# Kernel tuning notes

Measured on AMD Instinct MI355X. Metric: run time of the kernel, lower is better.

Reference implementation:

```python
import jax, jax.numpy as jnp
import numpy as np

# Model dims (match init_kwargs)
HID = 1024   # hidden_size
H   = 16     # num_heads
DK  = 64     # head_dim (key)
DV  = 128    # head value dim = int(head_dim * expand_v)
VAL = H * DV # value_dim = 2048
CONV = 4     # short conv kernel size
EPS = 1e-6
NORM_EPS = 1e-5


def _causal_conv_silu(x, w):
    # x: [B,T,C], w: [C,K] depthwise causal conv, no bias, silu activation
    T = x.shape[1]
    K = w.shape[1]
    xp = jnp.pad(x, ((0, 0), (K - 1, 0), (0, 0)))
    y = sum(xp[:, i:i + T, :] * w[:, i] for i in range(K))
    return jax.nn.silu(y)


def setup_inputs() -> dict:
    key = jax.random.key(0)
    ks = jax.random.split(key, 16)
    s = 0.02
    rn = lambda k, sh: jax.random.normal(k, sh, jnp.float32)
    return {
        'hidden_states': rn(ks[0], (1, 2048, HID)),
        'norm_w': jnp.ones((HID,), jnp.float32),
        'q_w': rn(ks[1], (H * DK, HID)) * s,
        'k_w': rn(ks[2], (H * DK, HID)) * s,
        'v_w': rn(ks[3], (VAL, HID)) * s,
        'a_w': rn(ks[4], (H, HID)) * s,
        'b_w': rn(ks[5], (H, HID)) * s,
        'g_w': rn(ks[6], (VAL, HID)) * s,
        'dt_bias': jax.random.uniform(ks[7], (H,), jnp.float32, -2.0, 0.0),
        'A_log': jnp.log(jax.random.uniform(ks[8], (H,), jnp.float32, 1.0, 8.0)),
        'conv_q_w': rn(ks[9], (H * DK, CONV)) * 0.2,
        'conv_k_w': rn(ks[10], (H * DK, CONV)) * 0.2,
        'conv_v_w': rn(ks[11], (VAL, CONV)) * 0.2,
        'o_norm_w': jnp.ones((DV,), jnp.float32),
        'o_proj_w': rn(ks[12], (HID, VAL)) * s,
        'out_proj_w': rn(ks[13], (HID, HID)) * s,
    }


def reference(hidden_states, norm_w, q_w, k_w, v_w, a_w, b_w, g_w, dt_bias,
              A_log, conv_q_w, conv_k_w, conv_v_w, o_norm_w, o_proj_w, out_proj_w):
    B, T, D = hidden_states.shape
    # RMSNorm
    x = hidden_states * jax.lax.rsqrt(
        jnp.mean(hidden_states * hidden_states, -1, keepdims=True) + EPS) * norm_w

    # projections + causal depthwise short conv + silu
    q = _causal_conv_silu(x @ q_w.T, conv_q_w).reshape(B, T, H, DK)
    k = _causal_conv_silu(x @ k_w.T, conv_k_w).reshape(B, T, H, DK)
    v = _causal_conv_silu(x @ v_w.T, conv_v_w).reshape(B, T, H, DV)

    beta = jax.nn.sigmoid(x @ b_w.T)                       # [B,T,H]
    g = -jnp.exp(A_log) * jax.nn.softplus(x @ a_w.T + dt_bias)  # [B,T,H] log-decay

    # rank-1 DC removal on keys: (I - 1 1^T / DK) k, i.e. subtract per-head mean
    k = k - jnp.mean(k, -1, keepdims=True)

    # L2 normalize q, k along head dim; scale q
    q = q * jax.lax.rsqrt(jnp.sum(q * q, -1, keepdims=True) + EPS)
    k = k * jax.lax.rsqrt(jnp.sum(k * k, -1, keepdims=True) + EPS)
    q = q * (DK ** -0.5)

    # gated delta-rule recurrence over time (time-major scan)
    qT = q.transpose(1, 0, 2, 3)
    kT = k.transpose(1, 0, 2, 3)
    vT = v.transpose(1, 0, 2, 3)
    bT = beta.transpose(1, 0, 2)
    gT = g.transpose(1, 0, 2)

    def step(S, inp):
        qt, kt, vt, bt, gt = inp              # S: [B,H,DK,DV]
        S = S * jnp.exp(gt)[..., None, None]
        v_new = (vt - jnp.einsum('bhk,bhkv->bhv', kt, S)) * bt[..., None]
        S = S + jnp.einsum('bhk,bhv->bhkv', kt, v_new)
        o = jnp.einsum('bhk,bhkv->bhv', qt, S)
        return S, o

    S0 = jnp.zeros((B, H, DK, DV), x.dtype)
    _, oT = jax.lax.scan(step, S0, (qT, kT, vT, bT, gT))
    o = oT.transpose(1, 0, 2, 3)                           # [B,T,H,DV]

    # gated RMSNorm on output heads
    gate = (x @ g_w.T).reshape(B, T, H, DV)
    o = o * jax.lax.rsqrt(jnp.mean(o * o, -1, keepdims=True) + NORM_EPS) * o_norm_w
    o = o * jax.nn.silu(gate)

    o = o.reshape(B, T, VAL) @ o_proj_w.T                  # [B,T,HID]
    return o @ out_proj_w.T
```

## Files before the change

kernel.cpp:

```cpp
#include <hip/hip_runtime.h>
#include <math.h>

#define S72 72

typedef __bf16 bf16;
typedef __bf16 bf16x8 __attribute__((ext_vector_type(8)));
typedef __bf16 bf16x4v __attribute__((ext_vector_type(4)));
typedef __bf16 bf16x2v __attribute__((ext_vector_type(2)));
typedef float f32x4 __attribute__((ext_vector_type(4)));

__device__ __forceinline__ float wredsum(float v) {
#pragma unroll
  for (int off = 32; off > 0; off >>= 1) v += __shfl_xor(v, off, 64);
  return v;
}
__device__ __forceinline__ float sigmoidf_(float x) { return 1.f / (1.f + __expf(-x)); }

__device__ __forceinline__ int sxy(int row, int col) {
  return (row << 6) + ((((col >> 3) ^ (row & 7)) << 3) | (col & 7));
}
__device__ __forceinline__ int sx8(int row, int chunk) {
  return (row << 6) + ((chunk ^ (row & 7)) << 3);
}

__global__ __launch_bounds__(256) void k_pre(const float* __restrict__ h,
    const float* __restrict__ nw, const float* __restrict__ aw,
    const float* __restrict__ bw, const float* __restrict__ dtb,
    const float* __restrict__ alog, bf16* __restrict__ xb,
    float* __restrict__ graw, float* __restrict__ btb,
    const float* __restrict__ qw, const float* __restrict__ kw,
    const float* __restrict__ vw, const float* __restrict__ gw,
    const float* __restrict__ opw, const float* __restrict__ ow,
    bf16* qwb, bf16* kwb, bf16* vwb, bf16* gwb, bf16* opwb, bf16* owb) {
  __shared__ float red[4];
  __shared__ __align__(16) float xs[1024];
  int tid = threadIdx.x;
  if (blockIdx.x >= 2048) {
    long cb = blockIdx.x - 2048;
    for (long u = cb*256 + tid; u < 2359296; u += 4608l*256) {
      const float* src; bf16* dst; long l;
      if      (u <  262144) { src=qw;  dst=qwb;  l=u; }
      else if (u <  524288) { src=kw;  dst=kwb;  l=u-262144; }
      else if (u < 1048576) { src=vw;  dst=vwb;  l=u-524288; }
      else if (u < 1572864) { src=gw;  dst=gwb;  l=u-1048576; }
      else if (u < 2097152) { src=opw; dst=opwb; l=u-1572864; }
      else                  { src=ow;  dst=owb;  l=u-2097152; }
      float4 s = *(const float4*)(src + l*4);
      bf16x4v b; b[0]=(bf16)s.x; b[1]=(bf16)s.y; b[2]=(bf16)s.z; b[3]=(bf16)s.w;
      *(bf16x4v*)(dst + l*4) = b;
    }
    return;
  }
  int t = blockIdx.x;
  float4 hv = *(const float4*)(h + (size_t)t*1024 + tid*4);
  float ss = hv.x*hv.x + hv.y*hv.y + hv.z*hv.z + hv.w*hv.w;
  float wsum = wredsum(ss);
  if ((tid & 63) == 0) red[tid >> 6] = wsum;
  __syncthreads();
  float tot = red[0] + red[1] + red[2] + red[3];
  float rs = rsqrtf(tot * (1.f/1024.f) + 1e-6f);
  float4 w4 = *(const float4*)(nw + tid*4);
  float4 y;
  y.x = hv.x*rs*w4.x; y.y = hv.y*rs*w4.y; y.z = hv.z*rs*w4.z; y.w = hv.w*rs*w4.w;
  *(float4*)(xs + tid*4) = y;
  bf16x4v b; b[0]=(bf16)y.x; b[1]=(bf16)y.y; b[2]=(bf16)y.z; b[3]=(bf16)y.w;
  *(bf16x4v*)(xb + (size_t)t*1024 + tid*4) = b;
  __syncthreads();
  int wave = tid >> 6, lane = tid & 63;
  const float4* x4 = (const float4*)xs;
#pragma unroll
  for (int hi = 0; hi < 4; ++hi) {
    int hh = wave*4 + hi;
    float sa = 0.f, sb = 0.f;
#pragma unroll
    for (int i = 0; i < 4; ++i) {
      float4 xv = x4[i*64 + lane];
      float4 av = *(const float4*)(aw + hh*1024 + i*256 + lane*4);
      float4 bv = *(const float4*)(bw + hh*1024 + i*256 + lane*4);
      sa += xv.x*av.x + xv.y*av.y + xv.z*av.z + xv.w*av.w;
      sb += xv.x*bv.x + xv.y*bv.y + xv.z*bv.z + xv.w*bv.w;
    }
    sa = wredsum(sa); sb = wredsum(sb);
    if (lane == 0) {
      float ap = sa + dtb[hh];
      float sp = (ap > 20.f) ? ap : log1pf(expf(ap));
      graw[t*16 + hh] = -expf(alog[hh]) * sp;
      btb[t*16 + hh] = 1.f / (1.f + expf(-sb));
    }
  }
}

template <typename OutT>
__device__ __forceinline__ void gemm_body(const bf16* __restrict__ A,
    const bf16* __restrict__ B, OutT* __restrict__ C, int N, int K, int m0, int n0) {
  __shared__ bf16 As[2][128*32];
  __shared__ bf16 Bs[2][128*32];
  const int tid = threadIdx.x, lane = tid & 63, wave = tid >> 6;
  const int wm = (wave >> 1) * 64, wn = (wave & 1) * 64;
  const int srow = wave*16 + (lane >> 2);
  const int swl = (((lane & 3) ^ ((lane >> 3) & 3))) * 8;
  const int sdst = (lane & 3) * 8;
  const int quad = lane >> 4, l16 = lane & 15;
  const int sw = (l16 >> 1) & 3;
  f32x4 acc[4][4] = {};
  const int nk = K >> 5;
#pragma unroll
  for (int i = 0; i < 2; ++i) {
    int r = i*64 + srow;
    __builtin_amdgcn_global_load_lds(
      (__attribute__((address_space(1))) void*)(A + (size_t)(m0 + r)*K + swl),
      (__attribute__((address_space(3))) void*)(&As[0][r*32 + sdst]), 16, 0, 0);
    __builtin_amdgcn_global_load_lds(
      (__attribute__((address_space(1))) void*)(B + (size_t)(n0 + r)*K + swl),
      (__attribute__((address_space(3))) void*)(&Bs[0][r*32 + sdst]), 16, 0, 0);
  }
  for (int kt = 0; kt < nk; ++kt) {
    const int cur = kt & 1;
    __syncthreads();
    bf16x8 af[4], bfr[4];
#pragma unroll
    for (int mt = 0; mt < 4; ++mt)
      af[mt] = *(const bf16x8*)(&As[cur][(wm + mt*16 + l16)*32 + (quad ^ sw)*8]);
#pragma unroll
    for (int nt = 0; nt < 4; ++nt)
      bfr[nt] = *(const bf16x8*)(&Bs[cur][(wn + nt*16 + l16)*32 + (quad ^ sw)*8]);
    if (kt + 1 < nk) {
      int k0 = (kt + 1) << 5;
#pragma unroll
      for (int i = 0; i < 2; ++i) {
        int r = i*64 + srow;
        __builtin_amdgcn_global_load_lds(
          (__attribute__((address_space(1))) void*)(A + (size_t)(m0 + r)*K + k0 + swl),
          (__attribute__((address_space(3))) void*)(&As[cur^1][r*32 + sdst]), 16, 0, 0);
        __builtin_amdgcn_global_load_lds(
          (__attribute__((address_space(1))) void*)(B + (size_t)(n0 + r)*K + k0 + swl),
          (__attribute__((address_space(3))) void*)(&Bs[cur^1][r*32 + sdst]), 16, 0, 0);
      }
    }
#pragma unroll
    for (int mt = 0; mt < 4; ++mt)
#pragma unroll
      for (int nt = 0; nt < 4; ++nt)
        acc[mt][nt] = __builtin_amdgcn_mfma_f32_16x16x32_bf16(af[mt], bfr[nt], acc[mt][nt], 0, 0, 0);
  }
#pragma unroll
  for (int mt = 0; mt < 4; ++mt)
#pragma unroll
    for (int nt = 0; nt < 4; ++nt)
#pragma unroll
      for (int r = 0; r < 4; ++r) {
        int row = m0 + wm + mt*16 + quad*4 + r;
        int col = n0 + wn + nt*16 + l16;
        C[(size_t)row*N + col] = (OutT)acc[mt][nt][r];
      }
}

__global__ __launch_bounds__(256) void k_gemm_proj(const bf16* __restrict__ A,
    const bf16* __restrict__ qwb, const bf16* __restrict__ kwb,
    const bf16* __restrict__ vwb, const bf16* __restrict__ gwb,
    bf16* __restrict__ qpre, bf16* __restrict__ kpre,
    bf16* __restrict__ vpre, bf16* __restrict__ gpre) {
  int bx = blockIdx.x;
  const bf16* B; bf16* C; int N, xt;
  if      (bx <  8) { B = qwb; C = qpre; N = 1024; xt = bx; }
  else if (bx < 16) { B = kwb; C = kpre; N = 1024; xt = bx - 8; }
  else if (bx < 32) { B = vwb; C = vpre; N = 2048; xt = bx - 16; }
  else              { B = gwb; C = gpre; N = 2048; xt = bx - 32; }
  gemm_body<bf16>(A, B, C, N, 1024, blockIdx.y*128, xt*128);
}

template <typename OutT>
__global__ __launch_bounds__(256) void k_gemm_bt64(const bf16* __restrict__ A,
    const bf16* __restrict__ B, OutT* __restrict__ C, int N, int K) {
  __shared__ bf16 As[2][128*32];
  __shared__ bf16 Bs[2][64*32];
  const int tid = threadIdx.x, lane = tid & 63, wave = tid >> 6;
  const int wm = wave * 32;
  const int srow = wave*16 + (lane >> 2);
  const int swl = (((lane & 3) ^ ((lane >> 3) & 3))) * 8;
  const int sdst = (lane & 3) * 8;
  const int quad = lane >> 4, l16 = lane & 15;
  const int sw = (l16 >> 1) & 3;
  const int m0 = blockIdx.y * 128, n0 = blockIdx.x * 64;
  f32x4 acc[2][4] = {};
  const int nk = K >> 5;
#pragma unroll
  for (int i = 0; i < 2; ++i) {
    int r = i*64 + srow;
    __builtin_amdgcn_global_load_lds(
      (__attribute__((address_space(1))) void*)(A + (size_t)(m0 + r)*K + swl),
      (__attribute__((address_space(3))) void*)(&As[0][r*32 + sdst]), 16, 0, 0);
  }
  __builtin_amdgcn_global_load_lds(
    (__attribute__((address_space(1))) void*)(B + (size_t)(n0 + srow)*K + swl),
    (__attribute__((address_space(3))) void*)(&Bs[0][srow*32 + sdst]), 16, 0, 0);
  for (int kt = 0; kt < nk; ++kt) {
    const int cur = kt & 1;
    __syncthreads();
    bf16x8 af[2], bfr[4];
#pragma unroll
    for (int mt = 0; mt < 2; ++mt)
      af[mt] = *(const bf16x8*)(&As[cur][(wm + mt*16 + l16)*32 + (quad ^ sw)*8]);
#pragma unroll
    for (int nt = 0; nt < 4; ++nt)
      bfr[nt] = *(const bf16x8*)(&Bs[cur][(nt*16 + l16)*32 + (quad ^ sw)*8]);
    if (kt + 1 < nk) {
      int k0 = (kt + 1) << 5;
#pragma unroll
      for (int i = 0; i < 2; ++i) {
        int r = i*64 + srow;
        __builtin_amdgcn_global_load_lds(
          (__attribute__((address_space(1))) void*)(A + (size_t)(m0 + r)*K + k0 + swl),
          (__attribute__((address_space(3))) void*)(&As[cur^1][r*32 + sdst]), 16, 0, 0);
      }
      __builtin_amdgcn_global_load_lds(
        (__attribute__((address_space(1))) void*)(B + (size_t)(n0 + srow)*K + k0 + swl),
        (__attribute__((address_space(3))) void*)(&Bs[cur^1][srow*32 + sdst]), 16, 0, 0);
    }
#pragma unroll
    for (int mt = 0; mt < 2; ++mt)
#pragma unroll
      for (int nt = 0; nt < 4; ++nt)
        acc[mt][nt] = __builtin_amdgcn_mfma_f32_16x16x32_bf16(af[mt], bfr[nt], acc[mt][nt], 0, 0, 0);
  }
#pragma unroll
  for (int mt = 0; mt < 2; ++mt)
#pragma unroll
    for (int nt = 0; nt < 4; ++nt)
#pragma unroll
      for (int r = 0; r < 4; ++r) {
        int row = m0 + wm + mt*16 + quad*4 + r;
        int col = n0 + nt*16 + l16;
        C[(size_t)row*N + col] = (OutT)acc[mt][nt][r];
      }
}

template<int NT>
__device__ __forceinline__ void mm_band(const bf16* A_lds, const bf16* B_lds,
    int w16, int cb, int l16, int quad, f32x4* acc) {
#pragma unroll
  for (int n = 0; n < NT; ++n) { acc[n][0]=0.f; acc[n][1]=0.f; acc[n][2]=0.f; acc[n][3]=0.f; }
#pragma unroll
  for (int kt = 0; kt < 2; ++kt) {
    bf16x8 af = *(const bf16x8*)(A_lds + sx8(w16 + l16, kt*4 + quad));
#pragma unroll
    for (int n = 0; n < NT; ++n) {
      bf16x8 bf = *(const bf16x8*)(B_lds + sx8(cb + n*16 + l16, kt*4 + quad));
      acc[n] = __builtin_amdgcn_mfma_f32_16x16x32_bf16(af, bf, acc[n], 0, 0, 0);
    }
  }
}

__global__ __launch_bounds__(512, 4) void k_prepass(
    const bf16* __restrict__ qpre, const bf16* __restrict__ kpre,
    const bf16* __restrict__ vpre, const float* __restrict__ cqw,
    const float* __restrict__ ckw, const float* __restrict__ cvw,
    const float* __restrict__ graw, const float* __restrict__ beta,
    bf16* __restrict__ EF, float* __restrict__ dSl, float* __restrict__ obuf) {
  const int bx = blockIdx.x, c = bx >> 4, h = bx & 15, tid = threadIdx.x;
  const int t0 = c * 64;
  const int wave = tid >> 6, lane = tid & 63, l16 = lane & 15, quad = lane >> 4;
  const int w16 = (wave >> 1) * 16;
  const int chh = wave & 1;
  const int r0 = wave * 8;

  __shared__ bf16 SM[36864];
  __shared__ float bs[64], bts_s[64], es[64], gms[64];
  bf16* Kr    = SM;
  bf16* powR0 = SM + 4096;
  bf16* prod0 = SM + 8192;
  bf16* T2T   = SM + 12288;
  bf16* powT0 = SM + 16384;
  bf16* powR1 = SM + 20480;
  bf16* powT1 = SM + 24576;
  bf16* prod1 = SM + 28672;
  bf16* qbf   = SM + 32768;
  bf16* VT   = SM;
  bf16* VlT  = SM + 8192;
  bf16* KT   = powT0;
  bf16* KbT  = powR1;
  bf16* Pm   = powT1;
  bf16* WR   = prod0;
  bf16* Mrow = prod1;

  float4 wq  = *(const float4*)(cqw + (h*64 + lane)*4);
  float4 wk  = *(const float4*)(ckw + (h*64 + lane)*4);
  float4 wv0 = *(const float4*)(cvw + (h*128 + lane)*4);
  float4 wv1 = *(const float4*)(cvw + (h*128 + 64 + lane)*4);
  float qtv[11], ktv[11], vtv0[11], vtv1[11];
#pragma unroll
  for (int j = 0; j < 11; ++j) {
    int tg = t0 + r0 + j - 3;
    bool ok = tg >= 0;
    qtv[j]  = ok ? (float)qpre[(size_t)tg*1024 + h*64 + lane] : 0.f;
    ktv[j]  = ok ? (float)kpre[(size_t)tg*1024 + h*64 + lane] : 0.f;
    vtv0[j] = ok ? (float)vpre[(size_t)tg*2048 + h*128 + lane] : 0.f;
    vtv1[j] = ok ? (float)vpre[(size_t)tg*2048 + h*128 + 64 + lane] : 0.f;
  }

  if (tid < 64) {
    float g = graw[(size_t)(t0 + tid)*16 + h];
    float b = g;
#pragma unroll
    for (int off = 1; off < 64; off <<= 1) {
      float p = __shfl_up(b, off, 64);
      if (tid >= off) b += p;
    }
    bs[tid] = b;
    bts_s[tid] = beta[(size_t)(t0 + tid)*16 + h];
    float b63 = __shfl(b, 63, 64);
    es[tid] = __expf(b63 - b);
    gms[tid] = __expf(b);
  }

  float kreg[8], vreg[16];
  {
#pragma unroll
    for (int rr = 0; rr < 8; ++rr) {
      float y = qtv[rr]*wq.x + qtv[rr+1]*wq.y + qtv[rr+2]*wq.z + qtv[rr+3]*wq.w;
      y = y * sigmoidf_(y);
      float ssq = wredsum(y*y);
      y *= rsqrtf(ssq + 1e-6f) * 0.125f;
      qbf[sxy(r0+rr, lane)] = (bf16)y;
    }
#pragma unroll
    for (int rr = 0; rr < 8; ++rr) {
      float y = ktv[rr]*wk.x + ktv[rr+1]*wk.y + ktv[rr+2]*wk.z + ktv[rr+3]*wk.w;
      y = y * sigmoidf_(y);
      float s1 = y, s2 = y*y;
#pragma unroll
      for (int off = 32; off > 0; off >>= 1) {
        s1 += __shfl_xor(s1, off, 64);
        s2 += __shfl_xor(s2, off, 64);
      }
      float m = s1 * (1.f/64.f);
      float ssq = s2 - s1*m;
      y -= m;
      y *= rsqrtf(ssq + 1e-6f);
      kreg[rr] = y;
      Kr[sxy(r0+rr, lane)] = (bf16)y;
    }
#pragma unroll
    for (int rr = 0; rr < 8; ++rr) {
      float y0 = vtv0[rr]*wv0.x + vtv0[rr+1]*wv0.y + vtv0[rr+2]*wv0.z + vtv0[rr+3]*wv0.w;
      float y1 = vtv1[rr]*wv1.x + vtv1[rr+1]*wv1.y + vtv1[rr+2]*wv1.z + vtv1[rr+3]*wv1.w;
      vreg[rr]   = y0 * sigmoidf_(y0);
      vreg[8+rr] = y1 * sigmoidf_(y1);
    }
  }
  __syncthreads();

  {
    f32x4 acc[2];
    mm_band<2>(Kr, Kr, w16, chh*32, l16, quad, acc);
#pragma unroll
    for (int n = 0; n < 2; ++n) {
      int col = chh*32 + n*16 + l16;
      bf16x4v tv;
#pragma unroll
      for (int r = 0; r < 4; ++r) {
        int row = w16 + quad*4 + r;
        float nv = 0.f;
        if (row > col) nv = -bts_s[row] * __expf(bs[row] - bs[col]) * acc[n][r];
        bf16 nb = (bf16)nv;
        powR0[sxy(row, col)] = nb;
        tv[r] = nb;
        prod0[sxy(row, col)] = (row == col) ? (bf16)1.f : nb;
      }
      *(bf16x4v*)(powT0 + sxy(col, w16 + quad*4)) = tv;
    }
  }
  __syncthreads();

  int pc = 0, rc = 0;
#pragma unroll 1
  for (int i = 1; i <= 5; ++i) {
    bf16* sqA = pc ? powR1 : powR0;
    bf16* sqB = pc ? powT1 : powT0;
    bf16* sqRo = pc ? powR0 : powR1;
    bf16* sqTo = pc ? powT0 : powT1;
    {
      f32x4 acc[2];
      mm_band<2>(sqA, sqB, w16, chh*32, l16, quad, acc);
#pragma unroll
      for (int n = 0; n < 2; ++n) {
        int col = chh*32 + n*16 + l16;
        bf16x4v tv;
#pragma unroll
        for (int r = 0; r < 4; ++r) {
          int row = w16 + quad*4 + r;
          bf16 vb = (bf16)acc[n][r];
          sqRo[sxy(row, col)] = vb;
          tv[r] = vb;
        }
        *(bf16x4v*)(sqTo + sxy(col, w16 + quad*4)) = tv;
      }
    }
    __syncthreads();
    bf16* prA = rc ? prod1 : prod0;
    bf16* prO = rc ? prod0 : prod1;
    {
      f32x4 acc[2];
      mm_band<2>(prA, sqTo, w16, chh*32, l16, quad, acc);
#pragma unroll
      for (int n = 0; n < 2; ++n) {
        int col = chh*32 + n*16 + l16;
        bf16x4v tv;
#pragma unroll
        for (int r = 0; r < 4; ++r) {
          int row = w16 + quad*4 + r;
          float val = acc[n][r] + (float)prA[sxy(row, col)];
          prO[sxy(row, col)] = (bf16)val;
          tv[r] = (bf16)(val * bts_s[col] * gms[col]);
        }
        if (i == 5) *(bf16x4v*)(T2T + sxy(col, w16 + quad*4)) = tv;
      }
    }
    __syncthreads();
    pc ^= 1; rc ^= 1;
  }

#pragma unroll
  for (int rr = 0; rr < 8; ++rr) {
    KT[sxy(lane, r0+rr)]  = (bf16)kreg[rr];
    KbT[sxy(lane, r0+rr)] = (bf16)(kreg[rr] * es[r0+rr]);
  }
  {
    f32x4 acc[2];
#pragma unroll
    for (int n = 0; n < 2; ++n) { acc[n][0]=0.f; acc[n][1]=0.f; acc[n][2]=0.f; acc[n][3]=0.f; }
#pragma unroll
    for (int kt = 0; kt < 2; ++kt) {
      bf16x8 af = *(const bf16x8*)(qbf + sx8(w16 + l16, kt*4 + quad));
#pragma unroll
      for (int n = 0; n < 2; ++n) {
        bf16x8 bf = *(const bf16x8*)(Kr + sx8(chh*32 + n*16 + l16, kt*4 + quad));
        acc[n] = __builtin_amdgcn_mfma_f32_16x16x32_bf16(af, bf, acc[n], 0, 0, 0);
      }
    }
#pragma unroll
    for (int n = 0; n < 2; ++n) {
      int col = chh*32 + n*16 + l16;
#pragma unroll
      for (int r = 0; r < 4; ++r) {
        int row = w16 + quad*4 + r;
        float pv = (row >= col) ? __expf(bs[row] - bs[col]) * acc[n][r] : 0.f;
        Pm[sxy(row, col)] = (bf16)pv;
      }
    }
  }
  __syncthreads();

  {
    f32x4 acc[2];
    mm_band<2>(KbT, T2T, w16, chh*32, l16, quad, acc);
#pragma unroll
    for (int n = 0; n < 2; ++n) {
      int col = chh*32 + n*16 + l16;
#pragma unroll
      for (int r = 0; r < 4; ++r)
        WR[sxy(w16 + quad*4 + r, col)] = (bf16)acc[n][r];
    }
  }
#pragma unroll
  for (int hf = 0; hf < 2; ++hf)
#pragma unroll
    for (int rr = 0; rr < 8; ++rr)
      VT[sxy(hf*64 + lane, r0+rr)] = (bf16)(bts_s[r0+rr] * vreg[hf*8+rr]);
  __syncthreads();
  {
    f32x4 acc[2];
    mm_band<2>(WR, KT, w16, chh*32, l16, quad, acc);
    float gC = gms[63];
    size_t eb = (size_t)bx * 13824;
#pragma unroll
    for (int n = 0; n < 2; ++n) {
      int col = chh*32 + n*16 + l16;
#pragma unroll
      for (int r = 0; r < 4; ++r) {
        int row = w16 + quad*4 + r;
        float ev = ((row == col) ? gC : 0.f) - acc[n][r];
        bf16 eh = (bf16)ev;
        EF[eb + row*S72 + col] = eh;
        EF[eb + 4608 + row*S72 + col] = (bf16)(ev - (float)eh);
      }
    }
  }
  __syncthreads();
  {
    f32x4 acc[2];
    mm_band<2>(Pm, T2T, w16, chh*32, l16, quad, acc);
#pragma unroll
    for (int n = 0; n < 2; ++n) {
      int col = chh*32 + n*16 + l16;
#pragma unroll
      for (int r = 0; r < 4; ++r)
        WR[sxy(w16 + quad*4 + r, col)] = (bf16)acc[n][r];
    }
  }
  __syncthreads();
  {
    f32x4 acc[2];
    mm_band<2>(WR, KT, w16, chh*32, l16, quad, acc);
    size_t eb = (size_t)bx * 13824;
#pragma unroll
    for (int n = 0; n < 2; ++n) {
      int col = chh*32 + n*16 + l16;
#pragma unroll
      for (int r = 0; r < 4; ++r) {
        int row = w16 + quad*4 + r;
        float qv = (float)qbf[sxy(row, col)];
        EF[eb + 9216 + row*S72 + col] = (bf16)(gms[row]*qv - acc[n][r]);
      }
    }
  }
  __syncthreads();
  {
    f32x4 acc[4];
    mm_band<4>(Mrow, VT, w16, chh*64, l16, quad, acc);
#pragma unroll
    for (int n = 0; n < 4; ++n) {
      int col = chh*64 + n*16 + l16;
      bf16x4v tv;
#pragma unroll
      for (int r = 0; r < 4; ++r) tv[r] = (bf16)acc[n][r];
      *(bf16x4v*)(VlT + sxy(col, w16 + quad*4)) = tv;
    }
  }
  __syncthreads();
  {
    f32x4 acc[4];
    mm_band<4>(KbT, VlT, w16, chh*64, l16, quad, acc);
#pragma unroll
    for (int n = 0; n < 4; ++n) {
      int col = chh*64 + n*16 + l16;
#pragma unroll
      for (int r = 0; r < 4; ++r)
        dSl[(size_t)bx*8192 + (size_t)(w16 + quad*4 + r)*128 + col] = acc[n][r];
    }
  }
  {
    f32x4 acc[4];
    mm_band<4>(Pm, VlT, w16, chh*64, l16, quad, acc);
#pragma unroll
    for (int n = 0; n < 4; ++n) {
      int col = chh*64 + n*16 + l16;
#pragma unroll
      for (int r = 0; r < 4; ++r)
        obuf[(size_t)(t0 + w16 + quad*4 + r)*2048 + h*128 + col] = acc[n][r];
    }
  }
}

#define SEQ_LOAD(Cn, EHx, ELx, FFx, DSx)                                        \
  {                                                                             \
    const bf16* base_ = EF + (size_t)((Cn)*16 + h)*13824 + arow;                \
    _Pragma("unroll")                                                           \
    for (int kt = 0; kt < 2; ++kt) {                                            \
      EHx[kt] = *(const bf16x8*)(base_ + kt*32);                                \
      ELx[kt] = *(const bf16x8*)(base_ + 4608 + kt*32);                         \
      FFx[kt] = *(const bf16x8*)(base_ + 9216 + kt*32);                         \
    }                                                                           \
    const float* db_ = dSl + (size_t)((Cn)*16 + h)*8192 + drow;                 \
    _Pragma("unroll")                                                           \
    for (int nt = 0; nt < 2; ++nt)                                              \
      _Pragma("unroll")                                                         \
      for (int r = 0; r < 4; ++r)                                               \
        DSx[nt*4+r] = db_[(size_t)r*128 + nt*16];                               \
  }

#define SEQ_STEP(Cc, EHc, ELc, FFc, DSc, EHn, ELn, FFn, DSn, SRC, DST)          \
  {                                                                             \
    bf16x8 bh[2][2], bl[2][2];                                                  \
    _Pragma("unroll")                                                           \
    for (int nt = 0; nt < 2; ++nt)                                              \
      _Pragma("unroll")                                                         \
      for (int kt = 0; kt < 2; ++kt) {                                          \
        bh[nt][kt] = *(const bf16x8*)(&Sthi[SRC][(nt*16 + l16)*S72 + kt*32 + quad*8]); \
        bl[nt][kt] = *(const bf16x8*)(&Stlo[SRC][(nt*16 + l16)*S72 + kt*32 + quad*8]); \
      }                                                                         \
    if ((Cc) + 1 < 32) SEQ_LOAD((Cc) + 1, EHn, ELn, FFn, DSn);                  \
    f32x4 a1[2], a2[2], a3[2], o1[2], o2[2];                                    \
    _Pragma("unroll")                                                           \
    for (int nt = 0; nt < 2; ++nt)                                              \
      _Pragma("unroll")                                                         \
      for (int r = 0; r < 4; ++r) {                                             \
        a1[nt][r] = DSc[nt*4+r];                                                \
        a2[nt][r] = 0.f; a3[nt][r] = 0.f; o1[nt][r] = 0.f; o2[nt][r] = 0.f;     \
      }                                                                         \
    _Pragma("unroll")                                                           \
    for (int kt = 0; kt < 2; ++kt)                                              \
      _Pragma("unroll")                                                         \
      for (int nt = 0; nt < 2; ++nt) {                                          \
        a1[nt] = __builtin_amdgcn_mfma_f32_16x16x32_bf16(EHc[kt], bh[nt][kt], a1[nt], 0, 0, 0); \
        a2[nt] = __builtin_amdgcn_mfma_f32_16x16x32_bf16(EHc[kt], bl[nt][kt], a2[nt], 0, 0, 0); \
        a3[nt] = __builtin_amdgcn_mfma_f32_16x16x32_bf16(ELc[kt], bh[nt][kt], a3[nt], 0, 0, 0); \
        o1[nt] = __builtin_amdgcn_mfma_f32_16x16x32_bf16(FFc[kt], bh[nt][kt], o1[nt], 0, 0, 0); \
        o2[nt] = __builtin_amdgcn_mfma_f32_16x16x32_bf16(FFc[kt], bl[nt][kt], o2[nt], 0, 0, 0); \
      }                                                                         \
    {                                                                           \
      int t0c = (Cc)*64;                                                        \
      _Pragma("unroll")                                                         \
      for (int nt = 0; nt < 2; ++nt)                                            \
        _Pragma("unroll")                                                       \
        for (int r = 0; r < 4; ++r)                                             \
          osb[(size_t)(t0c + mb + quad*4 + r)*2048 + h*128 + dq*32 + nt*16 + l16] \
            = o1[nt][r] + o2[nt][r];                                            \
    }                                                                           \
    _Pragma("unroll")                                                           \
    for (int nt = 0; nt < 2; ++nt) {                                            \
      bf16x4v hv, lv;                                                           \
      _Pragma("unroll")                                                         \
      for (int r = 0; r < 4; ++r) {                                             \
        float v = a1[nt][r] + a2[nt][r] + a3[nt][r];                            \
        bf16 hb = (bf16)v;                                                      \
        hv[r] = hb;                                                             \
        lv[r] = (bf16)(v - (float)hb);                                          \
      }                                                                         \
      *(bf16x4v*)(&Sthi[DST][(nt*16 + l16)*S72 + mb + quad*4]) = hv;            \
      *(bf16x4v*)(&Stlo[DST][(nt*16 + l16)*S72 + mb + quad*4]) = lv;            \
    }                                                                           \
    asm volatile("s_waitcnt lgkmcnt(0)" ::: "memory");                          \
    __builtin_amdgcn_s_barrier();                                               \
  }

__global__ __launch_bounds__(256) void k_seq(const bf16* __restrict__ EF,
    const float* __restrict__ dSl, float* __restrict__ osb) {
  const int bid = blockIdx.x;
  const int h = (bid & 7) + 8*((bid >> 3) & 1);
  const int dq = bid >> 4;
  const int tid = threadIdx.x, wave = tid >> 6, lane = tid & 63;
  const int l16 = lane & 15, quad = lane >> 4;
  const int mb = wave * 16;
  __shared__ bf16 Sthi[2][32*S72], Stlo[2][32*S72];
  for (int i = tid; i < 2304; i += 256) { Sthi[0][i] = (bf16)0.f; Stlo[0][i] = (bf16)0.f; }

  const size_t arow = (size_t)(mb + l16)*S72 + quad*8;
  const size_t drow = (size_t)dq*32 + (size_t)(mb + quad*4)*128 + l16;

  bf16x8 ehA[2], elA[2], ffA[2], ehB[2], elB[2], ffB[2];
  float dsA[8], dsB[8];

  SEQ_LOAD(0, ehA, elA, ffA, dsA);
  asm volatile("s_waitcnt lgkmcnt(0)" ::: "memory");
  __builtin_amdgcn_s_barrier();

#pragma unroll 1
  for (int c = 0; c < 32; c += 2) {
    SEQ_STEP(c,     ehA, elA, ffA, dsA, ehB, elB, ffB, dsB, 0, 1);
    SEQ_STEP(c + 1, ehB, elB, ffB, dsB, ehA, elA, ffA, dsA, 1, 0);
  }
}

__global__ __launch_bounds__(256) void k_gatenorm(const float* __restrict__ o,
    const float* __restrict__ os, const bf16* __restrict__ gpre,
    const float* __restrict__ onw, bf16* __restrict__ og) {
  int t = blockIdx.x, wave = threadIdx.x >> 6, lane = threadIdx.x & 63;
  float2 nw = *(const float2*)(onw + lane*2);
#pragma unroll
  for (int hi = 0; hi < 4; ++hi) {
    int hh = wave*4 + hi;
    size_t base = (size_t)t*2048 + hh*128 + lane*2;
    float2 o2 = *(const float2*)(o + base);
    float2 s2 = *(const float2*)(os + base);
    o2.x += s2.x; o2.y += s2.y;
    float ss = wredsum(o2.x*o2.x + o2.y*o2.y);
    float rs = rsqrtf(ss * (1.f/128.f) + 1e-5f);
    bf16x2v g2 = *(const bf16x2v*)(gpre + base);
    float g0 = (float)g2[0], g1 = (float)g2[1];
    float r0 = o2.x * rs * nw.x * (g0 * sigmoidf_(g0));
    float r1 = o2.y * rs * nw.y * (g1 * sigmoidf_(g1));
    bf16x2v b; b[0] = (bf16)r0; b[1] = (bf16)r1;
    *(bf16x2v*)(og + base) = b;
  }
}

extern "C" void kernel_launch(void* const* d_in, const int* in_sizes, int n_in,
                              void* d_out, int out_size, void* d_ws, size_t ws_size,
                              hipStream_t stream) {
  const float* hs   = (const float*)d_in[0];
  const float* nw   = (const float*)d_in[1];
  const float* qw   = (const float*)d_in[2];
  const float* kw   = (const float*)d_in[3];
  const float* vw   = (const float*)d_in[4];
  const float* aw   = (const float*)d_in[5];
  const float* bw   = (const float*)d_in[6];
  const float* gw   = (const float*)d_in[7];
  const float* dtb  = (const float*)d_in[8];
  const float* alog = (const float*)d_in[9];
  const float* cqw  = (const float*)d_in[10];
  const float* ckw  = (const float*)d_in[11];
  const float* cvw  = (const float*)d_in[12];
  const float* onw  = (const float*)d_in[13];
  const float* opw  = (const float*)d_in[14];
  const float* ow   = (const float*)d_in[15];
  float* out = (float*)d_out;

  char* p = (char*)d_ws;
  auto alloc = [&](size_t bytes) { char* r = p; p += (bytes + 255) & ~255ull; return r; };
  bf16*  xb    = (bf16*) alloc((size_t)2048*1024*2);
  bf16*  qwb   = (bf16*) alloc((size_t)1024*1024*2);
  bf16*  kwb   = (bf16*) alloc((size_t)1024*1024*2);
  bf16*  vwb   = (bf16*) alloc((size_t)2048*1024*2);
  bf16*  gwb   = (bf16*) alloc((size_t)2048*1024*2);
  bf16*  opwb  = (bf16*) alloc((size_t)1024*2048*2);
  bf16*  owb   = (bf16*) alloc((size_t)1024*1024*2);
  bf16*  qpre  = (bf16*) alloc((size_t)2048*1024*2);
  bf16*  kpre  = (bf16*) alloc((size_t)2048*1024*2);
  bf16*  vpre  = (bf16*) alloc((size_t)2048*2048*2);
  bf16*  gpre  = (bf16*) alloc((size_t)2048*2048*2);
  float* graw  = (float*)alloc((size_t)2048*16*4);
  float* btb   = (float*)alloc((size_t)2048*16*4);
  float* ob    = (float*)alloc((size_t)2048*2048*4);
  bf16*  ogb   = (bf16*) alloc((size_t)2048*2048*2);
  bf16*  h1b   = (bf16*) alloc((size_t)2048*1024*2);
  bf16*  EF    = (bf16*) alloc((size_t)512*13824*2);
  float* osb   = (float*)alloc((size_t)512*8192*4);
  float* dSl   = (float*)xb;

  k_pre<<<2048+4608, 256, 0, stream>>>(hs, nw, aw, bw, dtb, alog, xb, graw, btb,
                                       qw, kw, vw, gw, opw, ow,
                                       qwb, kwb, vwb, gwb, opwb, owb);
  k_gemm_proj<<<dim3(48,16,1), 256, 0, stream>>>(xb, qwb, kwb, vwb, gwb, qpre, kpre, vpre, gpre);
  k_prepass<<<512, 512, 0, stream>>>(qpre, kpre, vpre, cqw, ckw, cvw, graw, btb, EF, dSl, ob);
  k_seq<<<64, 256, 0, stream>>>(EF, dSl, osb);
  k_gatenorm<<<2048, 256, 0, stream>>>(ob, osb, gpre, onw, ogb);
  k_gemm_bt64<bf16><<<dim3(16,16,1), 256, 0, stream>>>(ogb, opwb, h1b, 1024, 2048);
  k_gemm_bt64<float><<<dim3(16,16,1), 256, 0, stream>>>(h1b, owb, out, 1024, 1024);
}
```

Measured before the change: 269.3 us.

## Rewrite projection GEMM with 256x256 tiles, 8 waves, ping-pong staged loads

Replaces the 128x128 projection GEMM with a 256x256-tile, 512-thread kernel using BK=64, XOR-swizzled LDS and a split schedule that interleaves A/B prefetch halves with MFMA quadrants under s_setprio and barriers. The block index is remapped so consecutive blocks share the same weight tile across M. This aims to raise arithmetic intensity and overlap global loads with MFMA work, at the cost of only 192 blocks (fewer than CUs times occupancy) and heavy register use for 32 accumulators per thread.

```diff
diff --git a/kernel.cpp b/kernel.cpp
--- a/kernel.cpp
+++ b/kernel.cpp
@@ -90,83 +90,143 @@
   }
 }
 
-template <typename OutT>
-__device__ __forceinline__ void gemm_body(const bf16* __restrict__ A,
-    const bf16* __restrict__ B, OutT* __restrict__ C, int N, int K, int m0, int n0) {
-  __shared__ bf16 As[2][128*32];
-  __shared__ bf16 Bs[2][128*32];
-  const int tid = threadIdx.x, lane = tid & 63, wave = tid >> 6;
-  const int wm = (wave >> 1) * 64, wn = (wave & 1) * 64;
-  const int srow = wave*16 + (lane >> 2);
-  const int swl = (((lane & 3) ^ ((lane >> 3) & 3))) * 8;
-  const int sdst = (lane & 3) * 8;
-  const int quad = lane >> 4, l16 = lane & 15;
-  const int sw = (l16 >> 1) & 3;
-  f32x4 acc[4][4] = {};
-  const int nk = K >> 5;
-#pragma unroll
-  for (int i = 0; i < 2; ++i) {
-    int r = i*64 + srow;
-    __builtin_amdgcn_global_load_lds(
-      (__attribute__((address_space(1))) void*)(A + (size_t)(m0 + r)*K + swl),
-      (__attribute__((address_space(3))) void*)(&As[0][r*32 + sdst]), 16, 0, 0);
-    __builtin_amdgcn_global_load_lds(
-      (__attribute__((address_space(1))) void*)(B + (size_t)(n0 + r)*K + swl),
-      (__attribute__((address_space(3))) void*)(&Bs[0][r*32 + sdst]), 16, 0, 0);
-  }
-  for (int kt = 0; kt < nk; ++kt) {
-    const int cur = kt & 1;
-    __syncthreads();
-    bf16x8 af[4], bfr[4];
-#pragma unroll
-    for (int mt = 0; mt < 4; ++mt)
-      af[mt] = *(const bf16x8*)(&As[cur][(wm + mt*16 + l16)*32 + (quad ^ sw)*8]);
-#pragma unroll
-    for (int nt = 0; nt < 4; ++nt)
-      bfr[nt] = *(const bf16x8*)(&Bs[cur][(wn + nt*16 + l16)*32 + (quad ^ sw)*8]);
-    if (kt + 1 < nk) {
-      int k0 = (kt + 1) << 5;
-#pragma unroll
-      for (int i = 0; i < 2; ++i) {
-        int r = i*64 + srow;
-        __builtin_amdgcn_global_load_lds(
-          (__attribute__((address_space(1))) void*)(A + (size_t)(m0 + r)*K + k0 + swl),
-          (__attribute__((address_space(3))) void*)(&As[cur^1][r*32 + sdst]), 16, 0, 0);
-        __builtin_amdgcn_global_load_lds(
-          (__attribute__((address_space(1))) void*)(B + (size_t)(n0 + r)*K + k0 + swl),
-          (__attribute__((address_space(3))) void*)(&Bs[cur^1][r*32 + sdst]), 16, 0, 0);
-      }
-    }
-#pragma unroll
-    for (int mt = 0; mt < 4; ++mt)
-#pragma unroll
-      for (int nt = 0; nt < 4; ++nt)
-        acc[mt][nt] = __builtin_amdgcn_mfma_f32_16x16x32_bf16(af[mt], bfr[nt], acc[mt][nt], 0, 0, 0);
-  }
-#pragma unroll
-  for (int mt = 0; mt < 4; ++mt)
-#pragma unroll
-    for (int nt = 0; nt < 4; ++nt)
-#pragma unroll
-      for (int r = 0; r < 4; ++r) {
-        int row = m0 + wm + mt*16 + quad*4 + r;
-        int col = n0 + wn + nt*16 + l16;
-        C[(size_t)row*N + col] = (OutT)acc[mt][nt][r];
-      }
-}
-
-__global__ __launch_bounds__(256) void k_gemm_proj(const bf16* __restrict__ A,
+#define PROJ_STAGE_HALF(BUF, MAT, HALF, GBASE)                                   \
+  { _Pragma("unroll")                                                            \
+    for (int rd_ = 0; rd_ < 2; ++rd_) {                                          \
+      int row_ = srow + rd_*64;                                                  \
+      __builtin_amdgcn_global_load_lds(                                          \
+        (__attribute__((address_space(1))) void*)((GBASE) + (size_t)row_*1024 + ((schk ^ (row_ & 7))*8)), \
+        (__attribute__((address_space(3))) void*)(&S[BUF][MAT][HALF][row_*64 + schk*8]), \
+        16, 0, 0);                                                               \
+    } }
+
+#define PROJ_LDA(BUF, MT, KS) \
+  (*(const bf16x8*)(&S[BUF][0][(wm + (MT)*16) >> 7][((wm + (MT)*16 + l16) & 127)*64 + ((((KS)*4 + quad) ^ (l16 & 7))*8)]))
+#define PROJ_LDB(BUF, NT, KS) \
+  (*(const bf16x8*)(&S[BUF][1][(wn + (NT)*16) >> 7][((wn + (NT)*16 + l16) & 127)*64 + ((((KS)*4 + quad) ^ (l16 & 7))*8)]))
+
+__global__ __launch_bounds__(512, 2) void k_gemm_proj(const bf16* __restrict__ A,
     const bf16* __restrict__ qwb, const bf16* __restrict__ kwb,
     const bf16* __restrict__ vwb, const bf16* __restrict__ gwb,
     bf16* __restrict__ qpre, bf16* __restrict__ kpre,
     bf16* __restrict__ vpre, bf16* __restrict__ gpre) {
-  int bx = blockIdx.x;
+  const int d = blockIdx.y * 24 + blockIdx.x;
+  const int by = d & 7, bx = d >> 3;
   const bf16* B; bf16* C; int N, xt;
-  if      (bx <  8) { B = qwb; C = qpre; N = 1024; xt = bx; }
-  else if (bx < 16) { B = kwb; C = kpre; N = 1024; xt = bx - 8; }
-  else if (bx < 32) { B = vwb; C = vpre; N = 2048; xt = bx - 16; }
-  else              { B = gwb; C = gpre; N = 2048; xt = bx - 32; }
-  gemm_body<bf16>(A, B, C, N, 1024, blockIdx.y*128, xt*128);
+  if      (bx <  4) { B = qwb; C = qpre; N = 1024; xt = bx; }
+  else if (bx <  8) { B = kwb; C = kpre; N = 1024; xt = bx - 4; }
+  else if (bx < 16) { B = vwb; C = vpre; N = 2048; xt = bx - 8; }
+  else              { B = gwb; C = gpre; N = 2048; xt = bx - 16; }
+  const int m0 = by * 256, n0 = xt * 256;
+
+  __shared__ bf16 S[2][2][2][128*64];
+
+  const int tid = threadIdx.x, lane = tid & 63, wave = tid >> 6;
+  const int l16 = lane & 15, quad = lane >> 4;
+  const int wm = (wave >> 2) * 128, wn = (wave & 3) * 64;
+  const int srow = tid >> 3, schk = tid & 7;
+
+  f32x4 acc[8][4] = {};
+
+  PROJ_STAGE_HALF(0, 0, 0, A + (size_t)m0*1024);
+  PROJ_STAGE_HALF(0, 0, 1, A + (size_t)(m0+128)*1024);
+  PROJ_STAGE_HALF(0, 1, 0, B + (size_t)n0*1024);
+  PROJ_STAGE_HALF(0, 1, 1, B + (size_t)(n0+128)*1024);
+  asm volatile("s_waitcnt vmcnt(0)" ::: "memory");
+  __builtin_amdgcn_sched_barrier(0);
+  __builtin_amdgcn_s_barrier();
+
+#pragma unroll 1
+  for (int kt = 0; kt < 16; ++kt) {
+    const int cur = kt & 1, nxt = cur ^ 1;
+    const bool pf = (kt + 1 < 16);
+    const size_t knext = (size_t)(kt + 1) * 64;
+    bf16x8 af[4][2], b0[2][2], b1[2][2];
+
+#pragma unroll
+    for (int m = 0; m < 4; ++m) { af[m][0] = PROJ_LDA(cur, m, 0); af[m][1] = PROJ_LDA(cur, m, 1); }
+#pragma unroll
+    for (int n = 0; n < 2; ++n) { b0[n][0] = PROJ_LDB(cur, n, 0); b0[n][1] = PROJ_LDB(cur, n, 1); }
+    if (pf) {
+      PROJ_STAGE_HALF(nxt, 0, 0, A + (size_t)m0*1024 + knext);
+      PROJ_STAGE_HALF(nxt, 0, 1, A + (size_t)(m0+128)*1024 + knext);
+    }
+    __builtin_amdgcn_s_barrier();
+    asm volatile("s_waitcnt lgkmcnt(0)" ::: "memory");
+    __builtin_amdgcn_sched_barrier(0);
+    __builtin_amdgcn_s_setprio(1);
+#pragma unroll
+    for (int ks = 0; ks < 2; ++ks)
+#pragma unroll
+      for (int m = 0; m < 4; ++m)
+#pragma unroll
+        for (int n = 0; n < 2; ++n)
+          acc[m][n] = __builtin_amdgcn_mfma_f32_16x16x32_bf16(af[m][ks], b0[n][ks], acc[m][n], 0, 0, 0);
+    __builtin_amdgcn_s_setprio(0);
+    __builtin_amdgcn_s_barrier();
+
+#pragma unroll
+    for (int n = 0; n < 2; ++n) { b1[n][0] = PROJ_LDB(cur, 2+n, 0); b1[n][1] = PROJ_LDB(cur, 2+n, 1); }
+    if (pf) {
+      PROJ_STAGE_HALF(nxt, 1, 0, B + (size_t)n0*1024 + knext);
+      PROJ_STAGE_HALF(nxt, 1, 1, B + (size_t)(n0+128)*1024 + knext);
+    }
+    __builtin_amdgcn_s_barrier();
+    asm volatile("s_waitcnt lgkmcnt(0)" ::: "memory");
+    __builtin_amdgcn_sched_barrier(0);
+    __builtin_amdgcn_s_setprio(1);
+#pragma unroll
+    for (int ks = 0; ks < 2; ++ks)
+#pragma unroll
+      for (int m = 0; m < 4; ++m)
+#pragma unroll
+        for (int n = 0; n < 2; ++n)
+          acc[m][2+n] = __builtin_amdgcn_mfma_f32_16x16x32_bf16(af[m][ks], b1[n][ks], acc[m][2+n], 0, 0, 0);
+    __builtin_amdgcn_s_setprio(0);
+    __builtin_amdgcn_s_barrier();
+
+#pragma unroll
+    for (int m = 0; m < 4; ++m) { af[m][0] = PROJ_LDA(cur, 4+m, 0); af[m][1] = PROJ_LDA(cur, 4+m, 1); }
+    __builtin_amdgcn_s_barrier();
+    asm volatile("s_waitcnt lgkmcnt(0)" ::: "memory");
+    __builtin_amdgcn_sched_barrier(0);
+    __builtin_amdgcn_s_setprio(1);
+#pragma unroll
+    for (int ks = 0; ks < 2; ++ks)
+#pragma unroll
+      for (int m = 0; m < 4; ++m)
+#pragma unroll
+        for (int n = 0; n < 2; ++n)
+          acc[4+m][2+n] = __builtin_amdgcn_mfma_f32_16x16x32_bf16(af[m][ks], b1[n][ks], acc[4+m][2+n], 0, 0, 0);
+    __builtin_amdgcn_s_setprio(0);
+    __builtin_amdgcn_s_barrier();
+
+    __builtin_amdgcn_s_setprio(1);
+#pragma unroll
+    for (int ks = 0; ks < 2; ++ks)
+#pragma unroll
+      for (int m = 0; m < 4; ++m)
+#pragma unroll
+        for (int n = 0; n < 2; ++n)
+          acc[4+m][n] = __builtin_amdgcn_mfma_f32_16x16x32_bf16(af[m][ks], b0[n][ks], acc[4+m][n], 0, 0, 0);
+    __builtin_amdgcn_s_setprio(0);
+    if (pf) {
+      asm volatile("s_waitcnt vmcnt(0)" ::: "memory");
+      __builtin_amdgcn_sched_barrier(0);
+    }
+    __builtin_amdgcn_s_barrier();
+  }
+
+#pragma unroll
+  for (int mt = 0; mt < 8; ++mt)
+#pragma unroll
+    for (int nt = 0; nt < 4; ++nt)
+#pragma unroll
+      for (int r = 0; r < 4; ++r) {
+        int row = m0 + wm + mt*16 + quad*4 + r;
+        int col = n0 + wn + nt*16 + l16;
+        C[(size_t)row*N + col] = (bf16)acc[mt][nt][r];
+      }
 }
 
 template <typename OutT>
@@ -721,7 +781,7 @@
   k_pre<<<2048+4608, 256, 0, stream>>>(hs, nw, aw, bw, dtb, alog, xb, graw, btb,
                                        qw, kw, vw, gw, opw, ow,
                                        qwb, kwb, vwb, gwb, opwb, owb);
-  k_gemm_proj<<<dim3(48,16,1), 256, 0, stream>>>(xb, qwb, kwb, vwb, gwb, qpre, kpre, vpre, gpre);
+  k_gemm_proj<<<dim3(24,8,1), 512, 0, stream>>>(xb, qwb, kwb, vwb, gwb, qpre, kpre, vpre, gpre);
   k_prepass<<<512, 512, 0, stream>>>(qpre, kpre, vpre, cqw, ckw, cvw, graw, btb, EF, dSl, ob);
   k_seq<<<64, 256, 0, stream>>>(EF, dSl, osb);
   k_gatenorm<<<2048, 256, 0, stream>>>(ob, osb, gpre, onw, ogb);
```

New measurement: 266.1 us. No clear change (-1.2%).
